# Optimization experiments

Measured on AMD Instinct MI355X. Metric: run time of the kernel, lower is better.

Reference implementation:

```python
import jax, jax.numpy as jnp
import numpy as np

N = 200000   # nodes
E = 600000   # edges (E*C = 76.8M floats gathered per layer -> memory bound)
C = 128      # channels
L = 2        # GNN layers
OUT = 1      # head out_channels
SEEDS = 1024


def setup_inputs() -> dict:
    key = jax.random.key(0)
    ks = jax.random.split(key, 8)
    s = 1.0 / np.sqrt(C)
    return {
        "x": jax.random.normal(ks[0], (N, C), jnp.float32),
        "node_time": jax.random.randint(ks[1], (N,), 0, 4),          # times in [0,4)
        "edge_index": jax.random.randint(ks[2], (2, E), 0, N),
        "w_root": jax.random.normal(ks[3], (L, C, C), jnp.float32) * s,
        "w_nbr": jax.random.normal(ks[4], (L, C, C), jnp.float32) * s,
        "bias": jnp.zeros((L, C), jnp.float32),
        "ln_g": jnp.ones((L, C), jnp.float32),
        "ln_b": jnp.zeros((L, C), jnp.float32),
        "head_w": jax.random.normal(ks[5], (C, OUT), jnp.float32) * s,
        "head_b": jnp.zeros((OUT,), jnp.float32),
        "min_timestamp": 0,
        "max_timestamp": 3,
        "update_period": 1,
        "num_seeds": SEEDS,
    }


def _layer_norm(h, g, b):
    mu = h.mean(-1, keepdims=True)
    var = h.var(-1, keepdims=True)
    return (h - mu) * jax.lax.rsqrt(var + 1e-5) * g + b


def reference(x, node_time, edge_index, w_root, w_nbr, bias, ln_g, ln_b,
              head_w, head_b, min_timestamp, max_timestamp, update_period, num_seeds):
    src, dst = edge_index[0], edge_index[1]
    n = x.shape[0]
    n_layers = w_root.shape[0]
    # edge introduction time = max of endpoint times (partition_edges_by_time_dict)
    intro = jnp.maximum(node_time[src], node_time[dst])
    periods = (intro - min_timestamp) // update_period
    P = (max_timestamp - min_timestamp + update_period) // update_period  # static int

    for p in range(P):
        emask = periods == p                     # [E] edges of this time period
        ef = emask.astype(x.dtype)
        ei = emask.astype(jnp.int32)
        # nodes involved in this period's subgraph (appear as src or dst of a period edge)
        cnt = jnp.zeros((n,), jnp.int32).at[src].add(ei).at[dst].add(ei)
        involved = cnt > 0                       # [N]
        # in-degree within the period subgraph (for mean aggregation)
        deg = jax.ops.segment_sum(ef, dst, num_segments=n)
        inv_deg = (1.0 / jnp.maximum(deg, 1.0))[:, None]
        # GraphSAGE on the period subgraph: masked edges == subgraph edges, and the
        # per-node (root/LayerNorm/ReLU) transforms agree with the extracted subgraph.
        h = x
        for l in range(n_layers):
            msg = h[src] * ef[:, None]                               # gather + mask
            agg = jax.ops.segment_sum(msg, dst, num_segments=n) * inv_deg
            h = h @ w_root[l] + agg @ w_nbr[l] + bias[l]
            h = _layer_norm(h, ln_g[l], ln_b[l])
            if l < n_layers - 1:
                h = jax.nn.relu(h)
        # x_dict[node_ids] += out_feats  (scatter-add restricted to involved nodes)
        x = x + jnp.where(involved[:, None], h, jnp.zeros((), x.dtype))

    # head: MLP(channels -> out_channels, num_layers=1) on the seed rows
    return x[:num_seeds] @ head_w + head_b
```

## Files before the change

### kernel.cpp

```cpp
#include <hip/hip_runtime.h>


#define CD 128

typedef __attribute__((ext_vector_type(8))) short s16x8;
typedef __attribute__((ext_vector_type(4))) float f32x4;

static __device__ __forceinline__ unsigned short f2bf(float f) {
  unsigned u = __float_as_uint(f);
  u += 0x7FFF + ((u >> 16) & 1);
  return (unsigned short)(u >> 16);
}
static __device__ __forceinline__ float bf2f(unsigned us) {
  return __uint_as_float(us << 16);
}
static __device__ __forceinline__ void acc8(float* a, uint4 v) {
  a[0] += bf2f(v.x & 0xffffu); a[1] += bf2f(v.x >> 16);
  a[2] += bf2f(v.y & 0xffffu); a[3] += bf2f(v.y >> 16);
  a[4] += bf2f(v.z & 0xffffu); a[5] += bf2f(v.z >> 16);
  a[6] += bf2f(v.w & 0xffffu); a[7] += bf2f(v.w >> 16);
}
static __device__ __forceinline__ s16x8 pack8(const float* a, float sc) {
  s16x8 r;
#pragma unroll
  for (int j = 0; j < 8; ++j) r[j] = (short)f2bf(a[j] * sc);
  return r;
}

__global__ __launch_bounds__(256) void histk(const int* __restrict__ ntime,
    const int* __restrict__ eidx, int* __restrict__ deg_pd,
    unsigned char* __restrict__ inv,
    const int* __restrict__ minp, const int* __restrict__ up, int N, int E) {
  int e = blockIdx.x * 256 + threadIdx.x;
  if (e >= E) return;
  int s = eidx[e], d = eidx[E + e];
  int ts = ntime[s], td = ntime[d];
  int m = ts > td ? ts : td;
  int p = (m - minp[0]) / up[0];
  atomicAdd(&deg_pd[p * N + d], 1);
  inv[(size_t)p * N + s] = 1;
  inv[(size_t)p * N + d] = 1;
}

__global__ __launch_bounds__(256) void compcnt(const unsigned char* __restrict__ inv,
    int* __restrict__ bcnt, int NB2, int N) {
  int i = blockIdx.x * 256 + threadIdx.x;
  int bits = 0;
  if (i < N)
    bits = (int)inv[i] | ((int)inv[N + i] << 1)
         | ((int)inv[2 * (size_t)N + i] << 2) | ((int)inv[3 * (size_t)N + i] << 3);
  int wv = threadIdx.x >> 6;
  int lane = threadIdx.x & 63;
  __shared__ int wcnt[4][4];
#pragma unroll
  for (int p = 0; p < 4; ++p) {
    unsigned long long m = __ballot((bits >> p) & 1);
    if (lane == 0) wcnt[p][wv] = __popcll(m);
  }
  __syncthreads();
  if (threadIdx.x < 4) {
    int p = threadIdx.x;
    bcnt[p * NB2 + blockIdx.x] = wcnt[p][0] + wcnt[p][1] + wcnt[p][2] + wcnt[p][3];
  }
}

__global__ __launch_bounds__(256) void compscat(const unsigned char* __restrict__ inv,
    const int* __restrict__ bcnt, const int* __restrict__ bexc,
    int* __restrict__ nlist, int* __restrict__ cidx, int* __restrict__ ncnt,
    int NB2, int N) {
  int i = blockIdx.x * 256 + threadIdx.x;
  int bits = 0;
  if (i < N)
    bits = (int)inv[i] | ((int)inv[N + i] << 1)
         | ((int)inv[2 * (size_t)N + i] << 2) | ((int)inv[3 * (size_t)N + i] << 3);
  if (blockIdx.x == 0 && threadIdx.x < 4) {
    int p = threadIdx.x;
    ncnt[p] = bexc[p * NB2 + NB2 - 1] + bcnt[p * NB2 + NB2 - 1] - bexc[p * NB2];
  }
  int wv = threadIdx.x >> 6;
  int lane = threadIdx.x & 63;
  unsigned long long lanes_below = (lane == 0) ? 0ull : ((~0ull) >> (64 - lane));
  __shared__ int wcnt[4][4];
  unsigned long long mm[4];
#pragma unroll
  for (int p = 0; p < 4; ++p) {
    mm[p] = __ballot((bits >> p) & 1);
    if (lane == 0) wcnt[p][wv] = __popcll(mm[p]);
  }
  __syncthreads();
#pragma unroll
  for (int p = 0; p < 4; ++p) {
    if (!((bits >> p) & 1)) continue;
    int wpre = (wv > 0 ? wcnt[p][0] : 0) + (wv > 1 ? wcnt[p][1] : 0)
             + (wv > 2 ? wcnt[p][2] : 0);
    int base = bexc[p * NB2 + blockIdx.x] - bexc[p * NB2];
    int pos = base + wpre + __popcll(mm[p] & lanes_below);
    nlist[p * N + pos] = i;
    cidx[p * N + i] = pos;
  }
}

__global__ __launch_bounds__(256) void scan1(const int* __restrict__ in,
    int* __restrict__ out, int* __restrict__ bsums, int M) {
  __shared__ int lds[256];
  int tid = threadIdx.x;
  int base = blockIdx.x * 1024 + tid * 4;
  int v0 = base + 0 < M ? in[base + 0] : 0;
  int v1 = base + 1 < M ? in[base + 1] : 0;
  int v2 = base + 2 < M ? in[base + 2] : 0;
  int v3 = base + 3 < M ? in[base + 3] : 0;
  int s = v0 + v1 + v2 + v3;
  lds[tid] = s;
  __syncthreads();
  for (int off = 1; off < 256; off <<= 1) {
    int t = tid >= off ? lds[tid - off] : 0;
    __syncthreads();
    lds[tid] += t;
    __syncthreads();
  }
  int run = lds[tid] - s;
  if (base + 0 < M) out[base + 0] = run; run += v0;
  if (base + 1 < M) out[base + 1] = run; run += v1;
  if (base + 2 < M) out[base + 2] = run; run += v2;
  if (base + 3 < M) out[base + 3] = run;
  if (tid == 255) bsums[blockIdx.x] = lds[255];
}

__global__ __launch_bounds__(256) void scan2(int* __restrict__ b, int M) {
  __shared__ int lds[256];
  int tid = threadIdx.x;
  int base = tid * 4;
  int v0 = base + 0 < M ? b[base + 0] : 0;
  int v1 = base + 1 < M ? b[base + 1] : 0;
  int v2 = base + 2 < M ? b[base + 2] : 0;
  int v3 = base + 3 < M ? b[base + 3] : 0;
  int s = v0 + v1 + v2 + v3;
  lds[tid] = s;
  __syncthreads();
  for (int off = 1; off < 256; off <<= 1) {
    int t = tid >= off ? lds[tid - off] : 0;
    __syncthreads();
    lds[tid] += t;
    __syncthreads();
  }
  int run = lds[tid] - s;
  if (base + 0 < M) b[base + 0] = run; run += v0;
  if (base + 1 < M) b[base + 1] = run; run += v1;
  if (base + 2 < M) b[base + 2] = run; run += v2;
  if (base + 3 < M) b[base + 3] = run;
}

__global__ __launch_bounds__(256) void scan3(int* __restrict__ out,
    const int* __restrict__ bsums, int M) {
  int add = bsums[blockIdx.x];
  int idx = blockIdx.x * 1024 + threadIdx.x;
#pragma unroll
  for (int k = 0; k < 4; ++k) {
    int i = idx + k * 256;
    if (i < M) out[i] += add;
  }
}

__global__ __launch_bounds__(256) void fillk(const int* __restrict__ ntime,
    const int* __restrict__ eidx, int* __restrict__ row_ptr, int* __restrict__ col,
    const int* __restrict__ minp, const int* __restrict__ up, int N, int E) {
  int e = blockIdx.x * 256 + threadIdx.x;
  if (e >= E) return;
  int s = eidx[e], d = eidx[E + e];
  int ts = ntime[s], td = ntime[d];
  int m = ts > td ? ts : td;
  int p = (m - minp[0]) / up[0];
  int pos = atomicAdd(&row_ptr[p * N + d], 1);
  col[pos] = s;
}

__global__ __launch_bounds__(256) void remapk(const int* __restrict__ col,
    int* __restrict__ col2, const int* __restrict__ cidx,
    const int* __restrict__ row_ptr, int N, int E) {
  int i = blockIdx.x * 256 + threadIdx.x;
  if (i >= E) return;
  int p = (i >= row_ptr[N - 1]) + (i >= row_ptr[2 * N - 1]) + (i >= row_ptr[3 * N - 1]);
  col2[i] = cidx[(size_t)p * N + col[i]];
}

__global__ __launch_bounds__(256) void wprep(const float* __restrict__ wroot,
    const float* __restrict__ wnbr, unsigned short* __restrict__ wt, int total) {
  int t = blockIdx.x * 256 + threadIdx.x;
  if (t >= total) return;
  int l = t >> 12;
  int rem = t & 4095;
  int q = rem >> 7;
  int n = rem & 127;
  const float* src = (q < 16) ? (wroot + l * CD * CD) : (wnbr + l * CD * CD);
  int qh = q & 15;
  unsigned short o[8];
#pragma unroll
  for (int j = 0; j < 8; ++j) {
    int kp = qh * 8 + j;
    int kt = (kp & 7) * 16 + (kp >> 3);
    o[j] = f2bf(src[kt * CD + n]);
  }
  uint4 pk;
  pk.x = (unsigned)o[0] | ((unsigned)o[1] << 16);
  pk.y = (unsigned)o[2] | ((unsigned)o[3] << 16);
  pk.z = (unsigned)o[4] | ((unsigned)o[5] << 16);
  pk.w = (unsigned)o[6] | ((unsigned)o[7] << 16);
  *(uint4*)(wt + (size_t)l * 32768 + ((size_t)q * CD + n) * 8) = pk;
}

__global__ __launch_bounds__(256) void xprep(const float* __restrict__ x,
    unsigned short* __restrict__ xb, float* __restrict__ x32, int nseed, int total) {
  int t = blockIdx.x * 256 + threadIdx.x;
  if (t >= total) return;
  int row = t >> 4, j = t & 15;
  const float* xp = x + (size_t)row * CD + j;
  bool seed = row < nseed;
  float* x3 = x32 + (size_t)row * CD + j;
  unsigned short o[8];
#pragma unroll
  for (int tt = 0; tt < 8; ++tt) {
    float v = xp[tt * 16];
    o[tt] = f2bf(v);
    if (seed) x3[tt * 16] = v;
  }
  uint4 pk;
  pk.x = (unsigned)o[0] | ((unsigned)o[1] << 16);
  pk.y = (unsigned)o[2] | ((unsigned)o[3] << 16);
  pk.z = (unsigned)o[4] | ((unsigned)o[5] << 16);
  pk.w = (unsigned)o[6] | ((unsigned)o[7] << 16);
  *(uint4*)(xb + (size_t)row * CD + j * 8) = pk;
}

__global__ __launch_bounds__(256, 2) void gemm_fused(
    const unsigned short* __restrict__ feat,
    const unsigned short* __restrict__ wt,
    const float* __restrict__ bias, const float* __restrict__ lng,
    const float* __restrict__ lnb,
    unsigned short* __restrict__ hout,
    float* __restrict__ x32, unsigned short* __restrict__ xbf,
    const int* __restrict__ nlp, const int* __restrict__ pcnt,
    const int* __restrict__ deg_pd, const int* __restrict__ row_ptr,
    const int* __restrict__ cols,
    int p, int N, int mode, int nseed) {
  int cnt = pcnt[0];
  int rbase = blockIdx.x * 128;
  if (rbase >= cnt) return;

  __shared__ unsigned short Blds[32768];
  {
    const uint4* src = (const uint4*)wt;
    uint4* dst = (uint4*)Blds;
#pragma unroll
    for (int i = 0; i < 16; ++i) dst[threadIdx.x + i * 256] = src[threadIdx.x + i * 256];
  }

  int tid = threadIdx.x;
  int w = tid >> 6;
  int lane = tid & 63;
  int l15 = lane & 15;
  int quad = lane >> 4;

  int dg_[2], st_[2];
  const unsigned short* b1[2];
#pragma unroll
  for (int rt = 0; rt < 2; ++rt) {
    int ii = rbase + w * 32 + rt * 16 + l15;
    ii = ii < cnt ? ii : cnt - 1;
    int node = nlp[ii];
    int key = p * N + node;
    int dg = deg_pd[key];
    dg_[rt] = dg;
    st_[rt] = row_ptr[key] - dg;
    b1[rt] = feat + (size_t)(mode == 0 ? node : ii) * CD;
  }

  s16x8 af[4][2][2];
#pragma unroll
  for (int kc = 0; kc < 2; ++kc)
#pragma unroll
    for (int ks = 0; ks < 2; ++ks) {
      int off = kc * 64 + (ks * 4 + quad) * 8;
#pragma unroll
      for (int rt = 0; rt < 2; ++rt)
        af[kc][ks][rt] = *(const s16x8*)(b1[rt] + off);
    }

  int cb = quad * 8;
#pragma unroll
  for (int rt = 0; rt < 2; ++rt) {
    float a0[8], a1[8], a2[8], a3[8];
#pragma unroll
    for (int j = 0; j < 8; ++j) { a0[j] = 0.f; a1[j] = 0.f; a2[j] = 0.f; a3[j] = 0.f; }
    int dg = dg_[rt], st = st_[rt];
    for (int j = 0; j < dg; ++j) {
      int r = cols[st + j];
      const unsigned short* rp = feat + (size_t)r * CD;
      uint4 v0 = *(const uint4*)(rp + cb);
      uint4 v1 = *(const uint4*)(rp + cb + 32);
      uint4 v2 = *(const uint4*)(rp + cb + 64);
      uint4 v3 = *(const uint4*)(rp + cb + 96);
      acc8(a0, v0); acc8(a1, v1); acc8(a2, v2); acc8(a3, v3);
    }
    float sc = dg > 0 ? 1.0f / (float)dg : 0.f;
    af[2][0][rt] = pack8(a0, sc);
    af[2][1][rt] = pack8(a1, sc);
    af[3][0][rt] = pack8(a2, sc);
    af[3][1][rt] = pack8(a3, sc);
  }

  __syncthreads();

  f32x4 acc[2][8];
#pragma unroll
  for (int rt = 0; rt < 2; ++rt)
#pragma unroll
    for (int ct = 0; ct < 8; ++ct) acc[rt][ct] = (f32x4)(0.f);

#pragma unroll
  for (int kc = 0; kc < 4; ++kc) {
#pragma unroll
    for (int ks = 0; ks < 2; ++ks) {
      int q = kc * 8 + ks * 4 + quad;
      s16x8 bfr[8];
#pragma unroll
      for (int ct = 0; ct < 8; ++ct)
        bfr[ct] = *(const s16x8*)&Blds[((size_t)q * CD + l15) * 8 + (size_t)ct * 128];
#pragma unroll
      for (int rt = 0; rt < 2; ++rt)
#pragma unroll
        for (int ct = 0; ct < 8; ++ct)
          acc[rt][ct] = __builtin_amdgcn_mfma_f32_16x16x32_bf16(
              af[kc][ks][rt], bfr[ct], acc[rt][ct], 0, 0, 0);
    }
  }

  float bb[8], gg[8], eb[8];
#pragma unroll
  for (int ct = 0; ct < 8; ++ct) {
    int c = ct * 16 + l15;
    bb[ct] = bias[c]; gg[ct] = lng[c]; eb[ct] = lnb[c];
  }
#pragma unroll
  for (int rt = 0; rt < 2; ++rt) {
#pragma unroll
    for (int reg = 0; reg < 4; ++reg) {
      int ridx = rbase + w * 32 + rt * 16 + quad * 4 + reg;
      float vals[8];
      float s = 0.f, ss = 0.f;
#pragma unroll
      for (int ct = 0; ct < 8; ++ct) {
        float v = acc[rt][ct][reg] + bb[ct];
        vals[ct] = v;
        s += v; ss += v * v;
      }
#pragma unroll
      for (int m = 1; m <= 8; m <<= 1) {
        s  += __shfl_xor(s, m, 64);
        ss += __shfl_xor(ss, m, 64);
      }
      float mu  = s * (1.0f / CD);
      float var = ss * (1.0f / CD) - mu * mu;
      float rs  = rsqrtf(var + 1e-5f);
      if (ridx < cnt) {
        float o[8];
#pragma unroll
        for (int ct = 0; ct < 8; ++ct) o[ct] = (vals[ct] - mu) * rs * gg[ct] + eb[ct];
        if (mode == 0) {
          uint4 pk;
          pk.x = (unsigned)f2bf(fmaxf(o[0], 0.f)) | ((unsigned)f2bf(fmaxf(o[1], 0.f)) << 16);
          pk.y = (unsigned)f2bf(fmaxf(o[2], 0.f)) | ((unsigned)f2bf(fmaxf(o[3], 0.f)) << 16);
          pk.z = (unsigned)f2bf(fmaxf(o[4], 0.f)) | ((unsigned)f2bf(fmaxf(o[5], 0.f)) << 16);
          pk.w = (unsigned)f2bf(fmaxf(o[6], 0.f)) | ((unsigned)f2bf(fmaxf(o[7], 0.f)) << 16);
          *(uint4*)(hout + (size_t)ridx * CD + l15 * 8) = pk;
        } else {
          int node = nlp[ridx];
          unsigned short* xp = xbf + (size_t)node * CD + l15 * 8;
          uint4 old = *(const uint4*)xp;
          float xn0 = bf2f(old.x & 0xffffu) + o[0], xn1 = bf2f(old.x >> 16) + o[1];
          float xn2 = bf2f(old.y & 0xffffu) + o[2], xn3 = bf2f(old.y >> 16) + o[3];
          float xn4 = bf2f(old.z & 0xffffu) + o[4], xn5 = bf2f(old.z >> 16) + o[5];
          float xn6 = bf2f(old.w & 0xffffu) + o[6], xn7 = bf2f(old.w >> 16) + o[7];
          uint4 pk;
          pk.x = (unsigned)f2bf(xn0) | ((unsigned)f2bf(xn1) << 16);
          pk.y = (unsigned)f2bf(xn2) | ((unsigned)f2bf(xn3) << 16);
          pk.z = (unsigned)f2bf(xn4) | ((unsigned)f2bf(xn5) << 16);
          pk.w = (unsigned)f2bf(xn6) | ((unsigned)f2bf(xn7) << 16);
          *(uint4*)xp = pk;
          if (node < nseed) {
            float* x3 = x32 + (size_t)node * CD + l15;
#pragma unroll
            for (int ct = 0; ct < 8; ++ct) x3[ct * 16] += o[ct];
          }
        }
      }
    }
  }
}

__global__ __launch_bounds__(256) void headk(const float* __restrict__ x,
    const float* __restrict__ hw, const float* __restrict__ hb,
    float* __restrict__ out, int seeds) {
  int wave = threadIdx.x >> 6;
  int lane = threadIdx.x & 63;
  int row = blockIdx.x * 4 + wave;
  if (row >= seeds) return;
  const float* xp = x + (size_t)row * CD;
  float v = xp[lane] * hw[lane] + xp[64 + lane] * hw[64 + lane];
#pragma unroll
  for (int m = 1; m < 64; m <<= 1) v += __shfl_xor(v, m, 64);
  if (lane == 0) out[row] = v + hb[0];
}

extern "C" void kernel_launch(void* const* d_in, const int* in_sizes, int n_in,
                              void* d_out, int out_size, void* d_ws, size_t ws_size,
                              hipStream_t stream) {
  const float* x     = (const float*)d_in[0];
  const int*   ntime = (const int*)d_in[1];
  const int*   eidx  = (const int*)d_in[2];
  const float* wroot = (const float*)d_in[3];
  const float* wnbr  = (const float*)d_in[4];
  const float* bias  = (const float*)d_in[5];
  const float* lng   = (const float*)d_in[6];
  const float* lnb   = (const float*)d_in[7];
  const float* headw = (const float*)d_in[8];
  const float* headb = (const float*)d_in[9];
  const int*   minp  = (const int*)d_in[10];
  const int*   up    = (const int*)d_in[12];

  int N = in_sizes[0] / CD;
  int E = in_sizes[2] / 2;
  const int P = 4;
  int M = P * N;
  int nseed = out_size;

  size_t off = 0;
  auto alloc = [&](size_t bytes) {
    void* p = (char*)d_ws + off;
    off += (bytes + 255) & ~(size_t)255;
    return p;
  };
  unsigned short* x_bf = (unsigned short*)alloc((size_t)N * CD * 2);
  unsigned short* h_bf = (unsigned short*)alloc((size_t)N * CD * 2);
  float*          x32  = (float*)alloc((size_t)nseed * CD * 4);
  unsigned short* wt   = (unsigned short*)alloc(2 * 32768 * 2);
  int* deg_pd   = (int*)alloc((size_t)M * 4);
  int* row_ptr  = (int*)alloc((size_t)M * 4);
  int* col      = (int*)alloc((size_t)E * 4);
  int* col2     = (int*)alloc((size_t)E * 4);
  unsigned char* inv = (unsigned char*)alloc((size_t)M);
  int* nlist    = (int*)alloc((size_t)M * 4);
  int* cidx     = (int*)alloc((size_t)M * 4);
  int* ncnt     = (int*)alloc(256);
  int* bsums    = (int*)alloc(4096);

  int NB2 = (N + 255) / 256;
  int M2 = 4 * NB2;
  int* bcnt = (int*)alloc((size_t)M2 * 4);
  int* bexc = (int*)alloc((size_t)M2 * 4);
  (void)ws_size;

  hipMemsetAsync(deg_pd, 0, (size_t)M * 4, stream);
  hipMemsetAsync(inv, 0, (size_t)M, stream);

  int egrid = (E + 255) / 256;
  int NB = (M + 1023) / 1024;
  int NBc = (M2 + 1023) / 1024;
  int ggrid = (N + 127) / 128;

  xprep<<<(N * 16 + 255) / 256, 256, 0, stream>>>(x, x_bf, x32, nseed, N * 16);
  wprep<<<(8192 + 255) / 256, 256, 0, stream>>>(wroot, wnbr, wt, 8192);
  histk<<<egrid, 256, 0, stream>>>(ntime, eidx, deg_pd, inv, minp, up, N, E);

  compcnt<<<NB2, 256, 0, stream>>>(inv, bcnt, NB2, N);
  scan1<<<NBc, 256, 0, stream>>>(bcnt, bexc, bsums, M2);
  scan2<<<1, 256, 0, stream>>>(bsums, NBc);
  scan3<<<NBc, 256, 0, stream>>>(bexc, bsums, M2);
  compscat<<<NB2, 256, 0, stream>>>(inv, bcnt, bexc, nlist, cidx, ncnt, NB2, N);

  scan1<<<NB, 256, 0, stream>>>(deg_pd, row_ptr, bsums, M);
  scan2<<<1, 256, 0, stream>>>(bsums, NB);
  scan3<<<NB, 256, 0, stream>>>(row_ptr, bsums, M);
  fillk<<<egrid, 256, 0, stream>>>(ntime, eidx, row_ptr, col, minp, up, N, E);
  remapk<<<egrid, 256, 0, stream>>>(col, col2, cidx, row_ptr, N, E);

  for (int p = 0; p < P; ++p) {
    const int* nlp = nlist + (size_t)p * N;
    const int* pc  = ncnt + p;
    gemm_fused<<<ggrid, 256, 0, stream>>>(x_bf, wt,
        bias, lng, lnb, h_bf, nullptr, nullptr, nlp, pc,
        deg_pd, row_ptr, col, p, N, 0, nseed);
    gemm_fused<<<ggrid, 256, 0, stream>>>(h_bf, wt + 32768,
        bias + CD, lng + CD, lnb + CD, nullptr, x32, x_bf, nlp, pc,
        deg_pd, row_ptr, col2, p, N, 1, nseed);
  }
  headk<<<(nseed + 3) / 4, 256, 0, stream>>>(x32, headw, headb, (float*)d_out, nseed);
}
```

Measured before the change: 621.0 us.

## Sort per-period involved-node lists by descending degree for load balancing

Adds a counting-sort pass (per-block histogram, scan, scatter) that reorders each period's involved-node list into 32 buckets by in-degree, highest degree first, and builds the compact index map from that order. The fused GEMM/aggregation kernels then process nodes grouped by similar degree, so heavy nodes are not mixed with light ones in the same tile. This aims to reduce wave divergence and tail imbalance in the gather loops. It costs five extra small kernel launches and extra index traffic in preprocessing, and it makes the layer-1 gathers through the remapped column indices less sequential.

Result: faster. 582.7 us (-6.2%).

```diff
diff --git a/kernel.cpp b/kernel.cpp
--- a/kernel.cpp
+++ b/kernel.cpp
@@ -66,7 +66,7 @@
 
 __global__ __launch_bounds__(256) void compscat(const unsigned char* __restrict__ inv,
     const int* __restrict__ bcnt, const int* __restrict__ bexc,
-    int* __restrict__ nlist, int* __restrict__ cidx, int* __restrict__ ncnt,
+    int* __restrict__ nlist, int* __restrict__ ncnt,
     int NB2, int N) {
   int i = blockIdx.x * 256 + threadIdx.x;
   int bits = 0;
@@ -96,7 +96,54 @@
     int base = bexc[p * NB2 + blockIdx.x] - bexc[p * NB2];
     int pos = base + wpre + __popcll(mm[p] & lanes_below);
     nlist[p * N + pos] = i;
-    cidx[p * N + i] = pos;
+  }
+}
+
+__global__ __launch_bounds__(256) void dhist(const int* __restrict__ nlist,
+    const int* __restrict__ ncnt, const int* __restrict__ deg_pd,
+    int* __restrict__ bcnt2, int NB2, int N) {
+  __shared__ int cnt[4][32];
+  int tid = threadIdx.x;
+  if (tid < 128) ((int*)cnt)[tid] = 0;
+  __syncthreads();
+  int gi = blockIdx.x * 256 + tid;
+#pragma unroll
+  for (int p = 0; p < 4; ++p) {
+    if (gi < ncnt[p]) {
+      int d = nlist[p * N + gi];
+      int dg = deg_pd[p * N + d];
+      int b = 31 - (dg < 31 ? dg : 31);
+      atomicAdd(&cnt[p][b], 1);
+    }
+  }
+  __syncthreads();
+  if (tid < 128) {
+    int p = tid >> 5, b = tid & 31;
+    bcnt2[(p * 32 + b) * NB2 + blockIdx.x] = cnt[p][b];
+  }
+}
+
+__global__ __launch_bounds__(256) void dscat(const int* __restrict__ nlist,
+    const int* __restrict__ ncnt, const int* __restrict__ deg_pd,
+    const int* __restrict__ bexc2, int* __restrict__ nlist2,
+    int* __restrict__ cidx2, int NB2, int N) {
+  __shared__ int cnt[4][32];
+  int tid = threadIdx.x;
+  if (tid < 128) ((int*)cnt)[tid] = 0;
+  __syncthreads();
+  int gi = blockIdx.x * 256 + tid;
+#pragma unroll
+  for (int p = 0; p < 4; ++p) {
+    if (gi < ncnt[p]) {
+      int node = nlist[p * N + gi];
+      int dg = deg_pd[p * N + node];
+      int b = 31 - (dg < 31 ? dg : 31);
+      int r = atomicAdd(&cnt[p][b], 1);
+      int base = bexc2[(p * 32 + b) * NB2 + blockIdx.x] - bexc2[p * 32 * NB2];
+      int pos = base + r;
+      nlist2[p * N + pos] = node;
+      cidx2[p * N + node] = pos;
+    }
   }
 }
 
@@ -449,14 +496,18 @@
   int* col2     = (int*)alloc((size_t)E * 4);
   unsigned char* inv = (unsigned char*)alloc((size_t)M);
   int* nlist    = (int*)alloc((size_t)M * 4);
-  int* cidx     = (int*)alloc((size_t)M * 4);
+  int* nlist2   = (int*)alloc((size_t)M * 4);
+  int* cidx2    = (int*)alloc((size_t)M * 4);
   int* ncnt     = (int*)alloc(256);
   int* bsums    = (int*)alloc(4096);
 
   int NB2 = (N + 255) / 256;
   int M2 = 4 * NB2;
-  int* bcnt = (int*)alloc((size_t)M2 * 4);
-  int* bexc = (int*)alloc((size_t)M2 * 4);
+  int M3 = 128 * NB2;
+  int* bcnt  = (int*)alloc((size_t)M2 * 4);
+  int* bexc  = (int*)alloc((size_t)M2 * 4);
+  int* bcnt2 = (int*)alloc((size_t)M3 * 4);
+  int* bexc2 = (int*)alloc((size_t)M3 * 4);
   (void)ws_size;
 
   hipMemsetAsync(deg_pd, 0, (size_t)M * 4, stream);
@@ -465,6 +516,7 @@
   int egrid = (E + 255) / 256;
   int NB = (M + 1023) / 1024;
   int NBc = (M2 + 1023) / 1024;
+  int NBd = (M3 + 1023) / 1024;
   int ggrid = (N + 127) / 128;
 
   xprep<<<(N * 16 + 255) / 256, 256, 0, stream>>>(x, x_bf, x32, nseed, N * 16);
@@ -475,16 +527,22 @@
   scan1<<<NBc, 256, 0, stream>>>(bcnt, bexc, bsums, M2);
   scan2<<<1, 256, 0, stream>>>(bsums, NBc);
   scan3<<<NBc, 256, 0, stream>>>(bexc, bsums, M2);
-  compscat<<<NB2, 256, 0, stream>>>(inv, bcnt, bexc, nlist, cidx, ncnt, NB2, N);
+  compscat<<<NB2, 256, 0, stream>>>(inv, bcnt, bexc, nlist, ncnt, NB2, N);
+
+  dhist<<<NB2, 256, 0, stream>>>(nlist, ncnt, deg_pd, bcnt2, NB2, N);
+  scan1<<<NBd, 256, 0, stream>>>(bcnt2, bexc2, bsums, M3);
+  scan2<<<1, 256, 0, stream>>>(bsums, NBd);
+  scan3<<<NBd, 256, 0, stream>>>(bexc2, bsums, M3);
+  dscat<<<NB2, 256, 0, stream>>>(nlist, ncnt, deg_pd, bexc2, nlist2, cidx2, NB2, N);
 
   scan1<<<NB, 256, 0, stream>>>(deg_pd, row_ptr, bsums, M);
   scan2<<<1, 256, 0, stream>>>(bsums, NB);
   scan3<<<NB, 256, 0, stream>>>(row_ptr, bsums, M);
   fillk<<<egrid, 256, 0, stream>>>(ntime, eidx, row_ptr, col, minp, up, N, E);
-  remapk<<<egrid, 256, 0, stream>>>(col, col2, cidx, row_ptr, N, E);
+  remapk<<<egrid, 256, 0, stream>>>(col, col2, cidx2, row_ptr, N, E);
 
   for (int p = 0; p < P; ++p) {
-    const int* nlp = nlist + (size_t)p * N;
+    const int* nlp = nlist2 + (size_t)p * N;
     const int* pc  = ncnt + p;
     gemm_fused<<<ggrid, 256, 0, stream>>>(x_bf, wt,
         bias, lng, lnb, h_bf, nullptr, nullptr, nlp, pc,
```
